# Performance work log

Hardware: AMD Instinct MI355X
Metric: run time of the kernel (lower is better)

The kernel has to match this reference:

```python
import jax, jax.numpy as jnp
import numpy as np
from jax import lax

NB_VERTICES = 2048  # init kwarg nb_vertices
N_POINTS = 524288


def setup_inputs() -> dict:
    key = jax.random.key(0)
    pos = jax.random.normal(key, (N_POINTS, 3), dtype=jnp.float32)
    return {"pos": pos}


def _fps_indices(pos, m):
    """Single-pass iterative farthest point sampling.
    pos: [N, 3] float. Returns int32 indices [m].
    Maintains a running min squared-distance buffer (classic FPS).
    """
    N = pos.shape[0]
    big = jnp.asarray(jnp.finfo(pos.dtype).max, pos.dtype)
    min_d = jnp.full((N,), big, dtype=pos.dtype)
    idxs = jnp.zeros((m,), dtype=jnp.int32)  # idxs[0] = 0 (deterministic start)

    def body(i, carry):
        min_d, idxs = carry
        last = jnp.take(pos, idxs[i - 1], axis=0)          # [3]
        d = jnp.sum((pos - last[None, :]) ** 2, axis=-1)    # [N]
        min_d = jnp.minimum(min_d, d)
        nxt = jnp.argmax(min_d).astype(jnp.int32)
        idxs = idxs.at[i].set(nxt)
        return (min_d, idxs)

    _, idxs = lax.fori_loop(1, m, body, (min_d, idxs))
    return idxs


@jax.jit
def _forward(pos):
    # ratio = nb_vertices / N  ->  fps returns ceil(N*ratio) = nb_vertices
    # indices in a single pass, so the original while-loop runs once.
    idxs = _fps_indices(pos, NB_VERTICES)
    return pos[idxs]  # [nb_vertices, 3]


def reference(pos):
    return _forward(pos)
```

## Files before the change

### kernel.cpp

```cpp
#include <hip/hip_runtime.h>
#include <float.h>


#define NPTS     524288
#define MOUT     2048
#define NBLK     64
#define NTHR     512
#define NWAVE    (NTHR / 64)
#define GTHREADS (NBLK * NTHR)
#define PPT      (NPTS / GTHREADS)
#define SLOT_STRIDE 8
#define MASK51   ((1ull << 51) - 1)


__global__ void __launch_bounds__(NTHR, 1) fps_kernel(
    const float* __restrict__ pos, float* __restrict__ out,
    unsigned long long* __restrict__ slots)
{
    const unsigned tid  = threadIdx.x;
    const unsigned lane = tid & 63u;
    const unsigned wav  = tid >> 6;
    const unsigned blk  = blockIdx.x;
    const unsigned g    = blk * NTHR + tid;

    float X[PPT], Y[PPT], Z[PPT], D[PPT];
#pragma unroll
    for (int p = 0; p < PPT; ++p) {
        const unsigned idx = g + (unsigned)p * GTHREADS;
        X[p] = pos[3u * idx + 0];
        Y[p] = pos[3u * idx + 1];
        Z[p] = pos[3u * idx + 2];
        D[p] = FLT_MAX;
    }

    float px = pos[0], py = pos[1], pz = pos[2];
    if (g == 0) { out[0] = px; out[1] = py; out[2] = pz; }

    __shared__ unsigned long long sred[2][NWAVE];

    for (int i = 1; i < MOUT; ++i) {
        float bv = -1.0f;
        unsigned bi = 0;
#pragma unroll
        for (int p = 0; p < PPT; ++p) {
            float dx = __fsub_rn(X[p], px);
            float dy = __fsub_rn(Y[p], py);
            float dz = __fsub_rn(Z[p], pz);
            float d  = __fadd_rn(__fadd_rn(__fmul_rn(dx, dx), __fmul_rn(dy, dy)),
                                 __fmul_rn(dz, dz));
            float m  = fminf(D[p], d);
            D[p] = m;
            if (m > bv) { bv = m; bi = g + (unsigned)p * GTHREADS; }
        }
        unsigned long long best =
            ((unsigned long long)__float_as_uint(bv) << 19) |
            (unsigned long long)((NPTS - 1u) - bi);

#pragma unroll
        for (int off = 32; off > 0; off >>= 1) {
            unsigned long long o = __shfl_xor(best, off, 64);
            if (o > best) best = o;
        }

        unsigned long long* sb = sred[i & 1];
        if (lane == 0) sb[wav] = best;
        __syncthreads();
        unsigned long long b2 = sb[lane & (NWAVE - 1u)];
#pragma unroll
        for (int off = NWAVE / 2; off > 0; off >>= 1) {
            unsigned long long o = __shfl_xor(b2, off, 64);
            if (o > b2) b2 = o;
        }

        unsigned long long* buf = slots + (unsigned)(i & 1) * (NBLK * SLOT_STRIDE);
        if (tid == 0) {
            __hip_atomic_store(&buf[blk * SLOT_STRIDE],
                               ((unsigned long long)i << 51) | b2,
                               __ATOMIC_RELAXED, __HIP_MEMORY_SCOPE_AGENT);
        }

        const unsigned long long tag = (unsigned long long)i;
        unsigned long long s;
        do {
            s = __hip_atomic_load(&buf[lane * SLOT_STRIDE],
                                  __ATOMIC_RELAXED, __HIP_MEMORY_SCOPE_AGENT);
            if ((s >> 51) == tag) break;
            __builtin_amdgcn_s_sleep(1);
        } while (true);
        unsigned long long c = s & MASK51;

        unsigned cidx = (NPTS - 1u) - (unsigned)(c & 0x7FFFFull);
        float cx = pos[3u * cidx + 0];
        float cy = pos[3u * cidx + 1];
        float cz = pos[3u * cidx + 2];

        unsigned long long win = c;
#pragma unroll
        for (int off = 32; off > 0; off >>= 1) {
            unsigned long long o = __shfl_xor(win, off, 64);
            if (o > win) win = o;
        }
        unsigned long long bal = __ballot(win == c);
        int src = __ffsll(bal) - 1;
        px = __shfl(cx, src, 64);
        py = __shfl(cy, src, 64);
        pz = __shfl(cz, src, 64);

        if (blk == 0 && tid == 0) {
            out[3 * i + 0] = px; out[3 * i + 1] = py; out[3 * i + 2] = pz;
        }
    }
}

extern "C" void kernel_launch(void* const* d_in, const int* in_sizes, int n_in,
                              void* d_out, int out_size, void* d_ws, size_t ws_size,
                              hipStream_t stream) {
    const float* pos = (const float*)d_in[0];
    float* out = (float*)d_out;
    unsigned long long* slots = (unsigned long long*)d_ws;

    void* args[] = { (void*)&pos, (void*)&out, (void*)&slots };
    hipLaunchCooperativeKernel((void*)fps_kernel, dim3(NBLK), dim3(NTHR),
                               args, 0, stream);
}
```

Baseline: 4.966 ms.

## Replace block barrier with tagged LDS flags and single-wave global exchange

Doubles threads per block to 1024, which halves points per thread. It replaces the per-iteration __syncthreads with tagged LDS slots that each wave publishes. Wave 0 alone polls those slots, does the cross-block global slot exchange, fetches the winner's coordinates and broadcasts them through tagged LDS words, while the other waves spin on LDS. This is meant to cut barrier and global polling traffic on the latency-bound serial loop, at the risk of spin contention and extra LDS polling by 15 waves.

```diff
diff --git a/kernel.cpp b/kernel.cpp
--- a/kernel.cpp
+++ b/kernel.cpp
@@ -5,7 +5,7 @@
 #define NPTS     524288
 #define MOUT     2048
 #define NBLK     64
-#define NTHR     512
+#define NTHR     1024
 #define NWAVE    (NTHR / 64)
 #define GTHREADS (NBLK * NTHR)
 #define PPT      (NPTS / GTHREADS)
@@ -37,8 +37,13 @@
     if (g == 0) { out[0] = px; out[1] = py; out[2] = pz; }
 
     __shared__ unsigned long long sred[2][NWAVE];
+    __shared__ unsigned long long bc[2][3];
+    if (tid < 2u * NWAVE) ((unsigned long long*)sred)[tid] = 0ull;
+    if (tid < 6u)         ((unsigned long long*)bc)[tid]   = 0ull;
+    __syncthreads();
 
     for (int i = 1; i < MOUT; ++i) {
+        const unsigned p2 = (unsigned)i & 1u;
         float bv = -1.0f;
         unsigned bi = 0;
 #pragma unroll
@@ -62,52 +67,69 @@
             if (o > best) best = o;
         }
 
-        unsigned long long* sb = sred[i & 1];
-        if (lane == 0) sb[wav] = best;
-        __syncthreads();
-        unsigned long long b2 = sb[lane & (NWAVE - 1u)];
-#pragma unroll
-        for (int off = NWAVE / 2; off > 0; off >>= 1) {
-            unsigned long long o = __shfl_xor(b2, off, 64);
-            if (o > b2) b2 = o;
-        }
-
-        unsigned long long* buf = slots + (unsigned)(i & 1) * (NBLK * SLOT_STRIDE);
-        if (tid == 0) {
-            __hip_atomic_store(&buf[blk * SLOT_STRIDE],
-                               ((unsigned long long)i << 51) | b2,
-                               __ATOMIC_RELAXED, __HIP_MEMORY_SCOPE_AGENT);
-        }
+        if (lane == 0)
+            __hip_atomic_store(&sred[p2][wav],
+                               ((unsigned long long)i << 51) | best,
+                               __ATOMIC_RELAXED, __HIP_MEMORY_SCOPE_WORKGROUP);
 
         const unsigned long long tag = (unsigned long long)i;
-        unsigned long long s;
-        do {
-            s = __hip_atomic_load(&buf[lane * SLOT_STRIDE],
-                                  __ATOMIC_RELAXED, __HIP_MEMORY_SCOPE_AGENT);
-            if ((s >> 51) == tag) break;
-            __builtin_amdgcn_s_sleep(1);
-        } while (true);
-        unsigned long long c = s & MASK51;
 
-        unsigned cidx = (NPTS - 1u) - (unsigned)(c & 0x7FFFFull);
-        float cx = pos[3u * cidx + 0];
-        float cy = pos[3u * cidx + 1];
-        float cz = pos[3u * cidx + 2];
+        if (wav == 0) {
+            unsigned long long e;
+            do {
+                e = __hip_atomic_load(&sred[p2][lane & (NWAVE - 1u)],
+                                      __ATOMIC_RELAXED, __HIP_MEMORY_SCOPE_WORKGROUP);
+            } while (!__all((e >> 51) == tag));
+            unsigned long long b2 = e & MASK51;
+#pragma unroll
+            for (int off = NWAVE / 2; off > 0; off >>= 1) {
+                unsigned long long o = __shfl_xor(b2, off, 64);
+                if (o > b2) b2 = o;
+            }
 
-        unsigned long long win = c;
+            unsigned long long* buf = slots + p2 * (NBLK * SLOT_STRIDE);
+            if (lane == 0)
+                __hip_atomic_store(&buf[blk * SLOT_STRIDE], (tag << 51) | b2,
+                                   __ATOMIC_RELAXED, __HIP_MEMORY_SCOPE_AGENT);
+
+            unsigned long long s;
+            do {
+                s = __hip_atomic_load(&buf[lane * SLOT_STRIDE],
+                                      __ATOMIC_RELAXED, __HIP_MEMORY_SCOPE_AGENT);
+            } while (!__all((s >> 51) == tag));
+
+            unsigned long long win = s & MASK51;
 #pragma unroll
-        for (int off = 32; off > 0; off >>= 1) {
-            unsigned long long o = __shfl_xor(win, off, 64);
-            if (o > win) win = o;
-        }
-        unsigned long long bal = __ballot(win == c);
-        int src = __ffsll(bal) - 1;
-        px = __shfl(cx, src, 64);
-        py = __shfl(cy, src, 64);
-        pz = __shfl(cz, src, 64);
-
-        if (blk == 0 && tid == 0) {
-            out[3 * i + 0] = px; out[3 * i + 1] = py; out[3 * i + 2] = pz;
+            for (int off = 32; off > 0; off >>= 1) {
+                unsigned long long o = __shfl_xor(win, off, 64);
+                if (o > win) win = o;
+            }
+            unsigned widx = (NPTS - 1u) - (unsigned)(win & 0x7FFFFull);
+            float x = pos[3u * widx + 0];
+            float y = pos[3u * widx + 1];
+            float z = pos[3u * widx + 2];
+            px = x; py = y; pz = z;
+            if (blk == 0 && lane == 0) {
+                out[3 * i + 0] = x; out[3 * i + 1] = y; out[3 * i + 2] = z;
+            }
+            if (lane < 3u) {
+                float c = (lane == 0) ? x : (lane == 1) ? y : z;
+                __hip_atomic_store(&bc[p2][lane],
+                                   (tag << 32) | (unsigned long long)__float_as_uint(c),
+                                   __ATOMIC_RELAXED, __HIP_MEMORY_SCOPE_WORKGROUP);
+            }
+        } else {
+            unsigned long long w0, w1, w2;
+            do {
+                w0 = __hip_atomic_load(&bc[p2][0], __ATOMIC_RELAXED, __HIP_MEMORY_SCOPE_WORKGROUP);
+                w1 = __hip_atomic_load(&bc[p2][1], __ATOMIC_RELAXED, __HIP_MEMORY_SCOPE_WORKGROUP);
+                w2 = __hip_atomic_load(&bc[p2][2], __ATOMIC_RELAXED, __HIP_MEMORY_SCOPE_WORKGROUP);
+                if ((w0 >> 32) == tag && (w1 >> 32) == tag && (w2 >> 32) == tag) break;
+                __builtin_amdgcn_s_sleep(1);
+            } while (true);
+            px = __uint_as_float((unsigned)(w0 & 0xFFFFFFFFull));
+            py = __uint_as_float((unsigned)(w1 & 0xFFFFFFFFull));
+            pz = __uint_as_float((unsigned)(w2 & 0xFFFFFFFFull));
         }
     }
 }
```

New measurement: 5.538 ms. 11.5% more time.
